# Kernel optimization log

Measured on AMD Instinct MI355X. Metric: run time of the kernel, lower is better.

## Reference

```python
import jax, jax.numpy as jnp
import numpy as np

DIM = 2048
N_HEADS = 16
N_KV_HEADS = 4
HEAD_DIM = 128
EPS = 1e-6
BS, SEQ = 2, 4096


def setup_inputs() -> dict:
    key = jax.random.key(0)
    ks = jax.random.split(key, 8)
    x = jax.random.normal(ks[0], (BS, SEQ, DIM), dtype=jnp.float32)
    # rotary freqs: unit-modulus complex represented as [seq, head_dim//2, 2]
    theta = 10000.0
    inv_freq = 1.0 / (theta ** (jnp.arange(0, HEAD_DIM, 2, dtype=jnp.float32) / HEAD_DIM))
    t = jnp.arange(SEQ, dtype=jnp.float32)
    ang = jnp.outer(t, inv_freq)  # [SEQ, HEAD_DIM//2]
    freqs_cis = jnp.stack([jnp.cos(ang), jnp.sin(ang)], axis=-1)  # [SEQ, HD/2, 2]
    std = 0.02
    wq = jax.random.normal(ks[1], (N_HEADS * HEAD_DIM, DIM), dtype=jnp.float32) * std
    wk = jax.random.normal(ks[2], (N_KV_HEADS * HEAD_DIM, DIM), dtype=jnp.float32) * std
    wv = jax.random.normal(ks[3], (N_KV_HEADS * HEAD_DIM, DIM), dtype=jnp.float32) * std
    wo = jax.random.normal(ks[4], (DIM, N_HEADS * HEAD_DIM), dtype=jnp.float32) * std
    q_norm_w = jnp.ones((HEAD_DIM,), dtype=jnp.float32)
    k_norm_w = jnp.ones((HEAD_DIM,), dtype=jnp.float32)
    return {"x": x, "freqs_cis": freqs_cis, "wq": wq, "wk": wk, "wv": wv,
            "wo": wo, "q_norm_w": q_norm_w, "k_norm_w": k_norm_w}


def _rms_norm(x, w, eps=EPS):
    xf = x.astype(jnp.float32)
    var = jnp.mean(xf * xf, axis=-1, keepdims=True)
    return w * (xf * jax.lax.rsqrt(var + eps)).astype(x.dtype)


def _apply_rope(x, freqs_cis):
    # x: [b, s, h, d]; freqs_cis: [s, d//2, 2] (cos, sin)
    b, s, h, d = x.shape
    xr = x.astype(jnp.float32).reshape(b, s, h, d // 2, 2)
    cos = freqs_cis[:s, :, 0][None, :, None, :]
    sin = freqs_cis[:s, :, 1][None, :, None, :]
    xre, xim = xr[..., 0], xr[..., 1]
    out = jnp.stack([xre * cos - xim * sin, xre * sin + xim * cos], axis=-1)
    return out.reshape(b, s, h, d).astype(x.dtype)


def reference(x, freqs_cis, wq, wk, wv, wo, q_norm_w, k_norm_w):
    bs, seqlen, _ = x.shape
    xq = jnp.einsum('bsd,ed->bse', x, wq).reshape(bs, seqlen, N_HEADS, HEAD_DIM)
    xk = jnp.einsum('bsd,ed->bse', x, wk).reshape(bs, seqlen, N_KV_HEADS, HEAD_DIM)
    xv = jnp.einsum('bsd,ed->bse', x, wv).reshape(bs, seqlen, N_KV_HEADS, HEAD_DIM)
    xq = _rms_norm(xq, q_norm_w)
    xk = _rms_norm(xk, k_norm_w)
    xq = _apply_rope(xq, freqs_cis)
    xk = _apply_rope(xk, freqs_cis)
    n_rep = N_HEADS // N_KV_HEADS
    # repeat_kv: [b,s,kvh,d] -> [b,s,kvh*n_rep,d]
    keys = jnp.repeat(xk, n_rep, axis=2)
    values = jnp.repeat(xv, n_rep, axis=2)
    q = xq.transpose(0, 2, 1, 3)  # [b,h,s,d]
    k = keys.transpose(0, 2, 1, 3)
    v = values.transpose(0, 2, 1, 3)
    scale = 1.0 / jnp.sqrt(jnp.asarray(HEAD_DIM, dtype=q.dtype))
    scores = jnp.einsum('bhqd,bhkd->bhqk', q, k) * scale
    causal = jnp.tril(jnp.ones((seqlen, seqlen), dtype=bool))
    scores = jnp.where(causal[None, None], scores, jnp.finfo(scores.dtype).min)
    attn = jax.nn.softmax(scores, axis=-1)
    out = jnp.einsum('bhqk,bhkd->bhqd', attn, v)
    out = out.transpose(0, 2, 1, 3).reshape(bs, seqlen, N_HEADS * HEAD_DIM)
    return jnp.einsum('bse,de->bsd', out, wo)
```

## Files before the change

kernel.cpp:

```cpp
#include <hip/hip_runtime.h>

typedef __bf16 bf16;
typedef __bf16 bf16x8 __attribute__((ext_vector_type(8)));
typedef __bf16 bf16x4 __attribute__((ext_vector_type(4)));
typedef __bf16 bf16x2 __attribute__((ext_vector_type(2)));
typedef float  f32x4  __attribute__((ext_vector_type(4)));

static_assert(sizeof(bf16x8) == 16, "bf16x8 must be 16B");

#define MFMA16(a, b, c) __builtin_amdgcn_mfma_f32_16x16x32_bf16((a), (b), (c), 0, 0, 0)

__device__ __forceinline__ void gload_lds16(const void* g, void* l) {
    __builtin_amdgcn_global_load_lds(
        (const __attribute__((address_space(1))) void*)(uintptr_t)g,
        (__attribute__((address_space(3))) void*)(uintptr_t)l,
        16, 0, 0);
}

__device__ __forceinline__ void cast8(const float* __restrict__ in, bf16* __restrict__ out, int i)
{
    const float4 a = ((const float4*)in)[i * 2];
    const float4 b = ((const float4*)in)[i * 2 + 1];
    bf16x8 o;
    o[0] = (bf16)a.x; o[1] = (bf16)a.y; o[2] = (bf16)a.z; o[3] = (bf16)a.w;
    o[4] = (bf16)b.x; o[5] = (bf16)b.y; o[6] = (bf16)b.z; o[7] = (bf16)b.w;
    ((bf16x8*)out)[i] = o;
}

__global__ __launch_bounds__(256)
void cast_all(const float* __restrict__ x,  const float* __restrict__ wq,
              const float* __restrict__ wk, const float* __restrict__ wv,
              bf16* __restrict__ xb, bf16* __restrict__ wb)
{
    const int blk = blockIdx.x;
    if (blk < 8192) {
        cast8(x, xb, blk * 256 + threadIdx.x);
    } else if (blk < 10240) {
        cast8(wq, wb, (blk - 8192) * 256 + threadIdx.x);
    } else if (blk < 10752) {
        cast8(wk, wb + 2048 * 2048, (blk - 10240) * 256 + threadIdx.x);
    } else {
        cast8(wv, wb + 2560 * 2048, (blk - 10752) * 256 + threadIdx.x);
    }
}

template <typename OT, bool FUSE_VT>
__global__ __launch_bounds__(256)
void gemm_bt(const bf16* __restrict__ A, const bf16* __restrict__ W,
             int K, int ldc, OT* __restrict__ C, bf16* __restrict__ vTp)
{
    __shared__ bf16 smem[2 * 128 * 64];
    bf16* As = smem;
    bf16* Bs = smem + 128 * 64;

    const int n0 = blockIdx.x * 128;
    const int m0 = blockIdx.y * 128;

    const int tid  = threadIdx.x;
    const int lane = tid & 63;
    const int wid  = tid >> 6;
    const int wm   = wid >> 1;
    const int wn   = wid & 1;
    const int quad = lane >> 4;
    const int l16  = lane & 15;
    const int key  = l16 & 7;

    const int srow  = wid * 32 + (lane >> 3);
    const int scolg = ((lane & 7) ^ (lane >> 3)) * 8;
    const bf16* ag = A + (size_t)(m0 + srow) * K + scolg;
    const bf16* wg = W + (size_t)(n0 + srow) * K + scolg;
    bf16* al = As + wid * 2048;
    bf16* bl = Bs + wid * 2048;

    f32x4 acc[4][4];
#pragma unroll
    for (int i = 0; i < 4; i++)
#pragma unroll
        for (int j = 0; j < 4; j++) acc[i][j] = f32x4{0.f, 0.f, 0.f, 0.f};

    for (int kt = 0; kt < K; kt += 64) {
        __syncthreads();
#pragma unroll
        for (int i = 0; i < 4; i++) {
            gload_lds16(ag + (size_t)(i * 8) * K, al + i * 8 * 64);
            gload_lds16(wg + (size_t)(i * 8) * K, bl + i * 8 * 64);
        }
        ag += 64; wg += 64;
        __syncthreads();

#pragma unroll
        for (int ks = 0; ks < 2; ks++) {
            bf16x8 af[4], bfv[4];
#pragma unroll
            for (int i = 0; i < 4; i++)
                af[i]  = *(const bf16x8*)(As + (wm * 64 + i * 16 + l16) * 64 + (((ks * 4 + quad) ^ key) * 8));
#pragma unroll
            for (int i = 0; i < 4; i++)
                bfv[i] = *(const bf16x8*)(Bs + (wn * 64 + i * 16 + l16) * 64 + (((ks * 4 + quad) ^ key) * 8));
#pragma unroll
            for (int mi = 0; mi < 4; mi++)
#pragma unroll
                for (int ni = 0; ni < 4; ni++)
                    acc[mi][ni] = MFMA16(af[mi], bfv[ni], acc[mi][ni]);
        }
    }

    if (FUSE_VT && n0 >= 2560) {
        __syncthreads();
        bf16* T = smem;
#pragma unroll
        for (int mi = 0; mi < 4; mi++) {
            const int scol = wm * 64 + mi * 16 + quad * 4;
            const int g    = scol >> 3;
            const int sub  = scol & 7;
#pragma unroll
            for (int ni = 0; ni < 4; ni++) {
                const int d = wn * 64 + ni * 16 + l16;
                bf16x4 h4;
                h4[0] = (bf16)acc[mi][ni][0]; h4[1] = (bf16)acc[mi][ni][1];
                h4[2] = (bf16)acc[mi][ni][2]; h4[3] = (bf16)acc[mi][ni][3];
                *(bf16x4*)(&T[d * 128 + ((g ^ (d & 7)) * 8 + sub)]) = h4;
            }
        }
        __syncthreads();
        const int kvh = (n0 - 2560) >> 7;
        const int bb  = m0 >> 12;
        bf16* vdst = vTp + ((size_t)((bb * 4 + kvh) * 128)) * 4096 + (m0 & 4095);
#pragma unroll
        for (int i = 0; i < 8; i++) {
            const int d = wid * 32 + i * 4 + quad;
            const bf16x8 v = *(const bf16x8*)(&T[d * 128 + ((l16 ^ (d & 7)) * 8)]);
            *(bf16x8*)(vdst + (size_t)d * 4096 + l16 * 8) = v;
        }
        return;
    }

#pragma unroll
    for (int mi = 0; mi < 4; mi++) {
        const int row = m0 + wm * 64 + mi * 16 + quad * 4;
#pragma unroll
        for (int ni = 0; ni < 4; ni++) {
            const int col = n0 + wn * 64 + ni * 16 + l16;
#pragma unroll
            for (int r = 0; r < 4; r++)
                C[(size_t)(row + r) * ldc + col] = (OT)acc[mi][ni][r];
        }
    }
}

__global__ __launch_bounds__(256)
void normrope_wo(bf16* __restrict__ qkv, const float* __restrict__ fc,
                 const float* __restrict__ qw, const float* __restrict__ kw,
                 const float* __restrict__ wo, bf16* __restrict__ wob)
{
    if (blockIdx.x >= 40960) {
        cast8(wo, wob, (blockIdx.x - 40960) * 256 + threadIdx.x);
        return;
    }
    const int row  = blockIdx.x * 4 + (threadIdx.x >> 6);
    const int lane = threadIdx.x & 63;
    const int slot = row % 20;
    const int tok  = row / 20;
    const int s    = tok & 4095;

    const float* w; int off; float post;
    if (slot < 16) { off = slot * 128;               w = qw; post = 0.12751681555f; }
    else           { off = 2048 + (slot - 16) * 128; w = kw; post = 1.0f; }

    bf16* p = qkv + (size_t)tok * 3072 + off;

    bf16x2 v = *(const bf16x2*)(p + 2 * lane);
    float x0 = (float)v[0], x1 = (float)v[1];

    float ss = x0 * x0 + x1 * x1;
    ss += __shfl_xor(ss, 1);  ss += __shfl_xor(ss, 2);  ss += __shfl_xor(ss, 4);
    ss += __shfl_xor(ss, 8);  ss += __shfl_xor(ss, 16); ss += __shfl_xor(ss, 32);
    const float r = rsqrtf(ss * (1.0f / 128.0f) + 1e-6f) * post;

    const float xn0 = x0 * r * w[2 * lane], xn1 = x1 * r * w[2 * lane + 1];

    const float2 cs = ((const float2*)fc)[(size_t)s * 64 + lane];
    const float c = cs.x, sn = cs.y;

    bf16x2 o;
    o[0] = (bf16)(xn0 * c - xn1 * sn);
    o[1] = (bf16)(xn0 * sn + xn1 * c);
    *(bf16x2*)(p + 2 * lane) = o;
}

__global__ __launch_bounds__(256, 2)
void flash(const bf16* __restrict__ qkv, const bf16* __restrict__ vT,
           bf16* __restrict__ out)
{
    const int bh  = blockIdx.y;
    const int b   = bh >> 4, h = bh & 15;
    const int kvh = h >> 2;

    const int tid  = threadIdx.x;
    const int lane = tid & 63;
    const int wid  = tid >> 6;
    const int quad = lane >> 4;
    const int l16  = lane & 15;
    const int key  = l16 & 7;

    __shared__ bf16 Ks[2][64 * 128];
    __shared__ bf16 Vs[128 * 64];
    __shared__ bf16 Ps[128 * 64];

    const bf16* kbase = qkv + (size_t)b * 4096 * 3072 + 2048 + kvh * 128;
    const bf16* vbase = vT + ((size_t)(b * 4 + kvh) * 128) * 4096;

    const int krow_off = lane >> 4;
    const int kcolg    = lane & 15;
    const int vrow_off = lane >> 3;
    const int vcolg    = lane & 7;

    for (int pass = 0; pass < 2; ++pass) {
        const int qt = pass ? (31 - blockIdx.x) : blockIdx.x;
        const int q0 = qt * 128;
        const int ntiles = qt * 2 + 2;

        __syncthreads();
#pragma unroll
        for (int i = 0; i < 4; i++) {
            const int r0 = wid * 16 + i * 4;
            const int rk = r0 + krow_off;
            const int gc = (kcolg ^ (rk & 7)) * 8;
            gload_lds16(kbase + (size_t)rk * 3072 + gc, &Ks[0][r0 * 128]);
        }

        bf16x8 qf[2][4];
        const bf16* qbase = qkv + ((size_t)(b * 4096 + q0 + wid * 32)) * 3072 + h * 128;
#pragma unroll
        for (int mt = 0; mt < 2; mt++)
#pragma unroll
            for (int ks = 0; ks < 4; ks++)
                qf[mt][ks] = *(const bf16x8*)(qbase + (size_t)(mt * 16 + l16) * 3072 + ks * 32 + quad * 8);

        f32x4 oacc[2][8];
#pragma unroll
        for (int mt = 0; mt < 2; mt++)
#pragma unroll
            for (int nd = 0; nd < 8; nd++) oacc[mt][nd] = f32x4{0.f, 0.f, 0.f, 0.f};
        float mrow[2], lrow[2];
#pragma unroll
        for (int mt = 0; mt < 2; mt++) { mrow[mt] = -__builtin_inff(); lrow[mt] = 0.f; }

        __syncthreads();

#pragma unroll
        for (int i = 0; i < 4; i++) {
            const int r0 = wid * 32 + i * 8;
            const int dv = r0 + vrow_off;
            const int gc = (vcolg ^ (dv & 7)) * 8;
            gload_lds16(vbase + (size_t)dv * 4096 + gc, &Vs[r0 * 64]);
        }
#pragma unroll
        for (int i = 0; i < 4; i++) {
            const int r0 = wid * 16 + i * 4;
            const int rk = r0 + krow_off;
            const int gc = (kcolg ^ (rk & 7)) * 8;
            gload_lds16(kbase + (size_t)(64 + rk) * 3072 + gc, &Ks[1][r0 * 128]);
        }

        f32x4 sA[2][4], sB[2][4];

        {
#pragma unroll
            for (int mt = 0; mt < 2; mt++)
#pragma unroll
                for (int nt = 0; nt < 4; nt++) sA[mt][nt] = f32x4{0.f, 0.f, 0.f, 0.f};
            __builtin_amdgcn_s_setprio(1);
#pragma unroll
            for (int ks = 0; ks < 4; ks++) {
                bf16x8 kf[4];
#pragma unroll
                for (int nt = 0; nt < 4; nt++)
                    kf[nt] = *(const bf16x8*)(&Ks[0][(nt * 16 + l16) * 128 + (((ks * 4 + quad) ^ key) * 8)]);
#pragma unroll
                for (int mt = 0; mt < 2; mt++)
#pragma unroll
                    for (int nt = 0; nt < 4; nt++)
                        sA[mt][nt] = MFMA16(kf[nt], qf[mt][ks], sA[mt][nt]);
            }
            __builtin_amdgcn_s_setprio(0);
        }

        auto step = [&](int t, f32x4 (&SA)[2][4], f32x4 (&SB)[2][4]) {
            const int kv0 = t * 64;

            if (kv0 + 63 > q0) {
#pragma unroll
                for (int mt = 0; mt < 2; mt++) {
                    const int qg = q0 + wid * 32 + mt * 16 + l16;
#pragma unroll
                    for (int nt = 0; nt < 4; nt++)
#pragma unroll
                        for (int r = 0; r < 4; r++) {
                            const int kvg = kv0 + nt * 16 + quad * 4 + r;
                            if (kvg > qg) SA[mt][nt][r] = -1e30f;
                        }
                }
            }

            float pm[2];
#pragma unroll
            for (int mt = 0; mt < 2; mt++) {
                float t8[8];
#pragma unroll
                for (int nt = 0; nt < 4; nt++) {
                    t8[2 * nt]     = fmaxf(SA[mt][nt][0], SA[mt][nt][1]);
                    t8[2 * nt + 1] = fmaxf(SA[mt][nt][2], SA[mt][nt][3]);
                }
                float m = fmaxf(fmaxf(fmaxf(t8[0], t8[1]), fmaxf(t8[2], t8[3])),
                                fmaxf(fmaxf(t8[4], t8[5]), fmaxf(t8[6], t8[7])));
                m = fmaxf(m, __shfl_xor(m, 16));
                m = fmaxf(m, __shfl_xor(m, 32));
                pm[mt] = m;
            }

            const bool rescale =
                !__all((pm[0] - mrow[0] <= 8.f) && (pm[1] - mrow[1] <= 8.f));
            if (rescale) {
#pragma unroll
                for (int mt = 0; mt < 2; mt++) {
                    const float mnew  = fmaxf(mrow[mt], pm[mt]);
                    const float alpha = exp2f(mrow[mt] - mnew);
                    mrow[mt] = mnew;
                    lrow[mt] *= alpha;
                    float ar[4];
#pragma unroll
                    for (int r = 0; r < 4; r++) ar[r] = __shfl(alpha, quad * 4 + r);
#pragma unroll
                    for (int nd = 0; nd < 8; nd++)
#pragma unroll
                        for (int r = 0; r < 4; r++) oacc[mt][nd][r] *= ar[r];
                }
            }

#pragma unroll
            for (int mt = 0; mt < 2; mt++) {
                const int prow = wid * 32 + mt * 16 + l16;
                float sn[4];
#pragma unroll
                for (int nt = 0; nt < 4; nt++) {
                    const float p0 = exp2f(SA[mt][nt][0] - mrow[mt]);
                    const float p1 = exp2f(SA[mt][nt][1] - mrow[mt]);
                    const float p2 = exp2f(SA[mt][nt][2] - mrow[mt]);
                    const float p3 = exp2f(SA[mt][nt][3] - mrow[mt]);
                    sn[nt] = (p0 + p1) + (p2 + p3);
                    bf16x4 h4;
                    h4[0] = (bf16)p0; h4[1] = (bf16)p1;
                    h4[2] = (bf16)p2; h4[3] = (bf16)p3;
                    const int g = (2 * nt + (quad >> 1)) ^ key;
                    *(bf16x4*)(&Ps[prow * 64 + g * 8 + (quad & 1) * 4]) = h4;
                }
                float s = (sn[0] + sn[1]) + (sn[2] + sn[3]);
                s += __shfl_xor(s, 16);
                s += __shfl_xor(s, 32);
                lrow[mt] += s;
            }

            __syncthreads();

            if (t + 1 < ntiles) {
#pragma unroll
                for (int mt = 0; mt < 2; mt++)
#pragma unroll
                    for (int nt = 0; nt < 4; nt++) SB[mt][nt] = f32x4{0.f, 0.f, 0.f, 0.f};
                __builtin_amdgcn_s_setprio(1);
#pragma unroll
                for (int ks = 0; ks < 4; ks++) {
                    bf16x8 kf[4];
#pragma unroll
                    for (int nt = 0; nt < 4; nt++)
                        kf[nt] = *(const bf16x8*)(&Ks[(t + 1) & 1][(nt * 16 + l16) * 128 + (((ks * 4 + quad) ^ key) * 8)]);
#pragma unroll
                    for (int mt = 0; mt < 2; mt++)
#pragma unroll
                        for (int nt = 0; nt < 4; nt++)
                            SB[mt][nt] = MFMA16(kf[nt], qf[mt][ks], SB[mt][nt]);
                }
                __builtin_amdgcn_s_setprio(0);
            }

            __builtin_amdgcn_s_setprio(1);
#pragma unroll
            for (int ks = 0; ks < 2; ks++) {
                bf16x8 pf[2];
#pragma unroll
                for (int mt = 0; mt < 2; mt++)
                    pf[mt] = *(const bf16x8*)(&Ps[(wid * 32 + mt * 16 + l16) * 64 + (((ks * 4 + quad) ^ key) * 8)]);
#pragma unroll
                for (int nd = 0; nd < 8; nd++) {
                    const bf16x8 vf = *(const bf16x8*)(&Vs[(nd * 16 + l16) * 64 + (((ks * 4 + quad) ^ key) * 8)]);
#pragma unroll
                    for (int mt = 0; mt < 2; mt++)
                        oacc[mt][nd] = MFMA16(pf[mt], vf, oacc[mt][nd]);
                }
            }
            __builtin_amdgcn_s_setprio(0);

            if (t + 1 < ntiles) {
                __syncthreads();
                const int kvv = (t + 1) * 64;
#pragma unroll
                for (int i = 0; i < 4; i++) {
                    const int r0 = wid * 32 + i * 8;
                    const int dv = r0 + vrow_off;
                    const int gc = (vcolg ^ (dv & 7)) * 8;
                    gload_lds16(vbase + (size_t)dv * 4096 + kvv + gc, &Vs[r0 * 64]);
                }
                if (t + 2 < ntiles) {
                    const int kvn = (t + 2) * 64;
#pragma unroll
                    for (int i = 0; i < 4; i++) {
                        const int r0 = wid * 16 + i * 4;
                        const int rk = r0 + krow_off;
                        const int gc = (kcolg ^ (rk & 7)) * 8;
                        gload_lds16(kbase + (size_t)(kvn + rk) * 3072 + gc, &Ks[t & 1][r0 * 128]);
                    }
                }
            }
        };

        for (int t = 0; t < ntiles; t += 2) {
            step(t,     sA, sB);
            step(t + 1, sB, sA);
        }

#pragma unroll
        for (int mt = 0; mt < 2; mt++) {
            const float inv = 1.0f / lrow[mt];
            float invr[4];
#pragma unroll
            for (int r = 0; r < 4; r++) invr[r] = __shfl(inv, quad * 4 + r);
#pragma unroll
            for (int r = 0; r < 4; r++) {
                const size_t srow = (size_t)(b * 4096 + q0 + wid * 32 + mt * 16 + quad * 4 + r);
#pragma unroll
                for (int nd = 0; nd < 8; nd++)
                    out[srow * 2048 + h * 128 + nd * 16 + l16] = (bf16)(oacc[mt][nd][r] * invr[r]);
            }
        }
    }
}

extern "C" void kernel_launch(void* const* d_in, const int* in_sizes, int n_in,
                              void* d_out, int out_size, void* d_ws, size_t ws_size,
                              hipStream_t stream)
{
    const float* x   = (const float*)d_in[0];
    const float* fc  = (const float*)d_in[1];
    const float* wq  = (const float*)d_in[2];
    const float* wk  = (const float*)d_in[3];
    const float* wv  = (const float*)d_in[4];
    const float* wo  = (const float*)d_in[5];
    const float* qnw = (const float*)d_in[6];
    const float* knw = (const float*)d_in[7];
    float* out = (float*)d_out;

    char* ws = (char*)d_ws;
    bf16* qkv = (bf16*)ws;
    bf16* vT  = (bf16*)(ws + 50331648);
    bf16* xb  = (bf16*)(ws + 58720256);
    bf16* att = xb;
    bf16* wb  = (bf16*)(ws + 92274688);
    bf16* wob = wb;

    cast_all<<<dim3(11264), 256, 0, stream>>>(x, wq, wk, wv, xb, wb);
    gemm_bt<bf16, true><<<dim3(24, 64), 256, 0, stream>>>(xb, wb, 2048, 3072, qkv, vT);
    normrope_wo<<<dim3(43008), 256, 0, stream>>>(qkv, fc, qnw, knw, wo, wob);
    flash<<<dim3(16, 32), 256, 0, stream>>>(qkv, vT, att);
    gemm_bt<float, false><<<dim3(16, 64), 256, 0, stream>>>(att, wob, 2048, 2048, out, nullptr);
}
```

Before: 635.8 us.

## Fuse RMSNorm and RoPE into QKV GEMM epilogue; remap flash blocks to XCDs

The QKV GEMM epilogue now stages each 128x128 Q/K tile in padded shared memory, applies per-head RMSNorm and RoPE there, and writes the result with coalesced 16-byte stores. This removes the separate normrope pass, which re-read and re-wrote the whole Q/K region of qkv. The wo cast moves into its own small kernel. The flash kernel also remaps block indices so blocks sharing a batch and KV head land on the same XCD, aiming for better L2 reuse of K/V; this depends on round-robin XCD dispatch.

```diff
diff --git a/kernel.cpp b/kernel.cpp
--- a/kernel.cpp
+++ b/kernel.cpp
@@ -44,14 +44,22 @@
     }
 }
 
-template <typename OT, bool FUSE_VT>
+__global__ __launch_bounds__(256)
+void cast_wo(const float* __restrict__ wo, bf16* __restrict__ wob)
+{
+    cast8(wo, wob, blockIdx.x * 256 + threadIdx.x);
+}
+
+template <typename OT, int FUSE>
 __global__ __launch_bounds__(256)
 void gemm_bt(const bf16* __restrict__ A, const bf16* __restrict__ W,
-             int K, int ldc, OT* __restrict__ C, bf16* __restrict__ vTp)
+             int K, int ldc, OT* __restrict__ C, bf16* __restrict__ vTp,
+             const float* __restrict__ fc, const float* __restrict__ qw,
+             const float* __restrict__ kw)
 {
-    __shared__ bf16 smem[2 * 128 * 64];
+    __shared__ bf16 smem[17408];
     bf16* As = smem;
-    bf16* Bs = smem + 128 * 64;
+    bf16* Bs = smem + 8192;
 
     const int n0 = blockIdx.x * 128;
     const int m0 = blockIdx.y * 128;
@@ -105,32 +113,96 @@
         }
     }
 
-    if (FUSE_VT && n0 >= 2560) {
-        __syncthreads();
+    if (FUSE) {
+        __syncthreads();
+        if (n0 >= 2560) {
+            bf16* T = smem;
+#pragma unroll
+            for (int mi = 0; mi < 4; mi++) {
+                const int scol = wm * 64 + mi * 16 + quad * 4;
+                const int g    = scol >> 3;
+                const int sub  = scol & 7;
+#pragma unroll
+                for (int ni = 0; ni < 4; ni++) {
+                    const int d = wn * 64 + ni * 16 + l16;
+                    bf16x4 h4;
+                    h4[0] = (bf16)acc[mi][ni][0]; h4[1] = (bf16)acc[mi][ni][1];
+                    h4[2] = (bf16)acc[mi][ni][2]; h4[3] = (bf16)acc[mi][ni][3];
+                    *(bf16x4*)(&T[d * 128 + ((g ^ (d & 7)) * 8 + sub)]) = h4;
+                }
+            }
+            __syncthreads();
+            const int kvh = (n0 - 2560) >> 7;
+            const int bb  = m0 >> 12;
+            bf16* vdst = vTp + ((size_t)((bb * 4 + kvh) * 128)) * 4096 + (m0 & 4095);
+#pragma unroll
+            for (int i = 0; i < 8; i++) {
+                const int d = wid * 32 + i * 4 + quad;
+                const bf16x8 v = *(const bf16x8*)(&T[d * 128 + ((l16 ^ (d & 7)) * 8)]);
+                *(bf16x8*)(vdst + (size_t)d * 4096 + l16 * 8) = v;
+            }
+            return;
+        }
+        const float* w   = (n0 < 2048) ? qw : kw;
+        const float post = (n0 < 2048) ? 0.12751681555f : 1.0f;
         bf16* T = smem;
 #pragma unroll
-        for (int mi = 0; mi < 4; mi++) {
-            const int scol = wm * 64 + mi * 16 + quad * 4;
-            const int g    = scol >> 3;
-            const int sub  = scol & 7;
+        for (int mi = 0; mi < 4; mi++)
 #pragma unroll
             for (int ni = 0; ni < 4; ni++) {
                 const int d = wn * 64 + ni * 16 + l16;
-                bf16x4 h4;
-                h4[0] = (bf16)acc[mi][ni][0]; h4[1] = (bf16)acc[mi][ni][1];
-                h4[2] = (bf16)acc[mi][ni][2]; h4[3] = (bf16)acc[mi][ni][3];
-                *(bf16x4*)(&T[d * 128 + ((g ^ (d & 7)) * 8 + sub)]) = h4;
-            }
-        }
-        __syncthreads();
-        const int kvh = (n0 - 2560) >> 7;
-        const int bb  = m0 >> 12;
-        bf16* vdst = vTp + ((size_t)((bb * 4 + kvh) * 128)) * 4096 + (m0 & 4095);
+#pragma unroll
+                for (int r = 0; r < 4; r++)
+                    T[(wm * 64 + mi * 16 + quad * 4 + r) * 136 + d] = (bf16)acc[mi][ni][r];
+            }
+        __syncthreads();
+
+        {
+            const int row  = tid >> 1;
+            const int half = tid & 1;
+            const int s    = (m0 + row) & 4095;
+            bf16* seg = T + row * 136 + half * 64;
+            bf16x8 v[8];
+            float ss = 0.f;
+#pragma unroll
+            for (int g = 0; g < 8; g++) {
+                v[g] = *(const bf16x8*)(seg + 8 * g);
+#pragma unroll
+                for (int e = 0; e < 8; e++) { const float f = (float)v[g][e]; ss += f * f; }
+            }
+            ss += __shfl_xor(ss, 1);
+            const float rr = rsqrtf(ss * (1.0f / 128.0f) + 1e-6f) * post;
+            const float* fcb = fc + (size_t)s * 128 + half * 64;
+            const float* wb2 = w + half * 64;
+#pragma unroll
+            for (int g = 0; g < 8; g++) {
+                const float4 fa = ((const float4*)(fcb + 8 * g))[0];
+                const float4 fb = ((const float4*)(fcb + 8 * g))[1];
+                const float4 wa = ((const float4*)(wb2 + 8 * g))[0];
+                const float4 wb4 = ((const float4*)(wb2 + 8 * g))[1];
+                const float cw[8] = {fa.x, fa.y, fa.z, fa.w, fb.x, fb.y, fb.z, fb.w};
+                const float ww[8] = {wa.x, wa.y, wa.z, wa.w, wb4.x, wb4.y, wb4.z, wb4.w};
+                bf16x8 o;
+#pragma unroll
+                for (int k = 0; k < 4; k++) {
+                    const float x0 = (float)v[g][2 * k]     * rr * ww[2 * k];
+                    const float x1 = (float)v[g][2 * k + 1] * rr * ww[2 * k + 1];
+                    const float c  = cw[2 * k], sn = cw[2 * k + 1];
+                    o[2 * k]     = (bf16)(x0 * c - x1 * sn);
+                    o[2 * k + 1] = (bf16)(x0 * sn + x1 * c);
+                }
+                *(bf16x8*)(seg + 8 * g) = o;
+            }
+        }
+        __syncthreads();
+
 #pragma unroll
         for (int i = 0; i < 8; i++) {
-            const int d = wid * 32 + i * 4 + quad;
-            const bf16x8 v = *(const bf16x8*)(&T[d * 128 + ((l16 ^ (d & 7)) * 8)]);
-            *(bf16x8*)(vdst + (size_t)d * 4096 + l16 * 8) = v;
+            const int flat = i * 256 + tid;
+            const int rrow = flat >> 4;
+            const int g    = flat & 15;
+            *(bf16x8*)((bf16*)C + (size_t)(m0 + rrow) * ldc + n0 + g * 8) =
+                *(const bf16x8*)(T + rrow * 136 + g * 8);
         }
         return;
     }
@@ -146,55 +218,19 @@
                 C[(size_t)(row + r) * ldc + col] = (OT)acc[mi][ni][r];
         }
     }
-}
-
-__global__ __launch_bounds__(256)
-void normrope_wo(bf16* __restrict__ qkv, const float* __restrict__ fc,
-                 const float* __restrict__ qw, const float* __restrict__ kw,
-                 const float* __restrict__ wo, bf16* __restrict__ wob)
-{
-    if (blockIdx.x >= 40960) {
-        cast8(wo, wob, (blockIdx.x - 40960) * 256 + threadIdx.x);
-        return;
-    }
-    const int row  = blockIdx.x * 4 + (threadIdx.x >> 6);
-    const int lane = threadIdx.x & 63;
-    const int slot = row % 20;
-    const int tok  = row / 20;
-    const int s    = tok & 4095;
-
-    const float* w; int off; float post;
-    if (slot < 16) { off = slot * 128;               w = qw; post = 0.12751681555f; }
-    else           { off = 2048 + (slot - 16) * 128; w = kw; post = 1.0f; }
-
-    bf16* p = qkv + (size_t)tok * 3072 + off;
-
-    bf16x2 v = *(const bf16x2*)(p + 2 * lane);
-    float x0 = (float)v[0], x1 = (float)v[1];
-
-    float ss = x0 * x0 + x1 * x1;
-    ss += __shfl_xor(ss, 1);  ss += __shfl_xor(ss, 2);  ss += __shfl_xor(ss, 4);
-    ss += __shfl_xor(ss, 8);  ss += __shfl_xor(ss, 16); ss += __shfl_xor(ss, 32);
-    const float r = rsqrtf(ss * (1.0f / 128.0f) + 1e-6f) * post;
-
-    const float xn0 = x0 * r * w[2 * lane], xn1 = x1 * r * w[2 * lane + 1];
-
-    const float2 cs = ((const float2*)fc)[(size_t)s * 64 + lane];
-    const float c = cs.x, sn = cs.y;
-
-    bf16x2 o;
-    o[0] = (bf16)(xn0 * c - xn1 * sn);
-    o[1] = (bf16)(xn0 * sn + xn1 * c);
-    *(bf16x2*)(p + 2 * lane) = o;
 }
 
 __global__ __launch_bounds__(256, 2)
 void flash(const bf16* __restrict__ qkv, const bf16* __restrict__ vT,
            bf16* __restrict__ out)
 {
-    const int bh  = blockIdx.y;
-    const int b   = bh >> 4, h = bh & 15;
-    const int kvh = h >> 2;
+    const int flat = blockIdx.y * 16 + blockIdx.x;
+    const int xcd  = flat & 7;
+    const int idx  = flat >> 3;
+    const int b    = xcd >> 2;
+    const int kvh  = xcd & 3;
+    const int h    = kvh * 4 + (idx >> 4);
+    const int bx   = idx & 15;
 
     const int tid  = threadIdx.x;
     const int lane = tid & 63;
@@ -216,7 +252,7 @@
     const int vcolg    = lane & 7;
 
     for (int pass = 0; pass < 2; ++pass) {
-        const int qt = pass ? (31 - blockIdx.x) : blockIdx.x;
+        const int qt = pass ? (31 - bx) : bx;
         const int q0 = qt * 128;
         const int ntiles = qt * 2 + 2;
 
@@ -469,8 +505,8 @@
     bf16* wob = wb;
 
     cast_all<<<dim3(11264), 256, 0, stream>>>(x, wq, wk, wv, xb, wb);
-    gemm_bt<bf16, true><<<dim3(24, 64), 256, 0, stream>>>(xb, wb, 2048, 3072, qkv, vT);
-    normrope_wo<<<dim3(43008), 256, 0, stream>>>(qkv, fc, qnw, knw, wo, wob);
+    gemm_bt<bf16, 1><<<dim3(24, 64), 256, 0, stream>>>(xb, wb, 2048, 3072, qkv, vT, fc, qnw, knw);
+    cast_wo<<<dim3(2048), 256, 0, stream>>>(wo, wob);
     flash<<<dim3(16, 32), 256, 0, stream>>>(qkv, vT, att);
-    gemm_bt<float, false><<<dim3(16, 64), 256, 0, stream>>>(att, wob, 2048, 2048, out, nullptr);
-}
+    gemm_bt<float, 0><<<dim3(16, 64), 256, 0, stream>>>(att, wob, 2048, 2048, out, nullptr, nullptr, nullptr, nullptr);
+}
```

Measured after the change: 683.6 us. 7.5% more time.
